# Optimization experiments

Hardware: AMD Instinct MI355X
Metric: run time of the kernel (lower is better)

Reference implementation:

```python
import jax, jax.numpy as jnp
from jax import lax
import numpy as np

B, C, H, W, O, K = 2, 64, 256, 256, 64, 3
STRIDE, DIL = 1, 1


def setup_inputs() -> dict:
    key = jax.random.key(0)
    ks = jax.random.split(key, 6)
    x = jax.random.normal(ks[0], (B, C, H, W), jnp.float32)
    # offset-predicting conv: 2*k^2 output channels (y,x per kernel tap)
    offset_w = jax.random.normal(ks[1], (2 * K * K, C, K, K), jnp.float32) * 0.01
    offset_b = jax.random.normal(ks[2], (2 * K * K,), jnp.float32) * 0.01
    # modulation conv: k^2 output channels
    amp_w = jax.random.normal(ks[3], (K * K, C, K, K), jnp.float32) * 0.01
    amp_b = jax.random.normal(ks[4], (K * K,), jnp.float32) * 0.01
    # conv3d weight [O, C, 1, 1, k^2] flattened to [O, C, k^2]
    w3d = jax.random.normal(ks[5], (O, C, K * K), jnp.float32) * (1.0 / np.sqrt(C * K * K))
    return {"x": x, "offset_w": offset_w, "offset_b": offset_b,
            "amp_w": amp_w, "amp_b": amp_b, "w3d": w3d}


def _conv2d(inp, w, b):
    out = lax.conv_general_dilated(inp, w, (STRIDE, STRIDE), 'VALID')
    return out + b[None, :, None, None]


def reference(x, offset_w, offset_b, amp_w, amp_b, w3d):
    k2 = K * K
    # 'same' padding as _pad_intput (k=3, s=1, d=1 -> pad 1 each side)
    pfs = K + (K - 1) * (DIL - 1)
    p = pfs - 1
    p0 = p // 2
    pad = jnp.pad(x, ((0, 0), (0, 0), (p0, p - p0), (p0, p - p0)))
    Bb, Cc, in_h, in_w = pad.shape

    off = _conv2d(pad, offset_w, offset_b)          # [B, 2k2, oh, ow]
    oh, ow = off.shape[2], off.shape[3]
    off = off.reshape(Bb, k2, 2, oh, ow).transpose(0, 3, 4, 1, 2)  # [B,oh,ow,k2,2]
    y_off, x_off = off[..., 0], off[..., 1]

    amp = jax.nn.sigmoid(_conv2d(pad, amp_w, amp_b))  # [B, k2, oh, ow]

    # base sampling grid (row-major over (ky,kx), as in nn.Unfold)
    ky, kx = jnp.meshgrid(jnp.arange(K), jnp.arange(K), indexing='ij')
    yb = (jnp.arange(oh) * STRIDE)[:, None] + (ky.reshape(-1) * DIL)[None, :]  # [oh,k2]
    xb = (jnp.arange(ow) * STRIDE)[:, None] + (kx.reshape(-1) * DIL)[None, :]  # [ow,k2]

    y = jnp.clip(yb[None, :, None, :].astype(jnp.float32) + y_off, 0, in_h - 1)
    xx = jnp.clip(xb[None, None, :, :].astype(jnp.float32) + x_off, 0, in_w - 1)
    y0 = jnp.floor(y)
    x0 = jnp.floor(xx)
    y1 = jnp.clip(y0 + 1, 0, in_h - 1)
    x1 = jnp.clip(x0 + 1, 0, in_w - 1)
    y0 = jnp.clip(y0, 0, in_h - 1)
    x0 = jnp.clip(x0, 0, in_w - 1)

    flat = pad.transpose(0, 2, 3, 1).reshape(Bb, in_h * in_w, Cc)

    def gather(yi, xi):
        idx = (yi.astype(jnp.int32) * in_w + xi.astype(jnp.int32)).reshape(Bb, -1)
        return jnp.take_along_axis(flat, idx[:, :, None], axis=1).reshape(Bb, oh, ow, k2, Cc)

    p0g = gather(y0, x0)
    p1g = gather(y0, x1)
    p2g = gather(y1, x0)
    p3g = gather(y1, x1)

    w0 = (y1 - y) * (x1 - xx)
    w1 = (y1 - y) * (xx - x0)
    w2 = (y - y0) * (x1 - xx)
    w3 = (y - y0) * (xx - x0)
    pixels = (w0[..., None] * p0g + w1[..., None] * p1g +
              w2[..., None] * p2g + w3[..., None] * p3g)   # [B,oh,ow,k2,C]

    # sigmoid modulation
    pixels = pixels * amp.transpose(0, 2, 3, 1)[..., None]

    # conv3d (1,1,k^2), no bias: contract over C and k^2
    out = jnp.einsum('bhwkc,ock->bohw', pixels, w3d)
    return jax.nn.relu(out)
```

## Files before the change

### kernel.cpp

```cpp
#include <hip/hip_runtime.h>
#include <hip/hip_bf16.h>
#include <math.h>

#define BB 2
#define CC 64
#define HH 256
#define WW 256
#define OO 64
#define K2 9
#define HW 65536
#define CHW (CC*HW)

typedef _Float16 h8 __attribute__((ext_vector_type(8)));
typedef __fp16 fp16x2 __attribute__((ext_vector_type(2)));
typedef __attribute__((ext_vector_type(4))) unsigned int ux4;
typedef __attribute__((ext_vector_type(4))) float f32x4;

__device__ __forceinline__ int xcd_swz(int bid, int nwg) {
    const int per = nwg >> 3;
    return (bid & 7) * per + (bid >> 3);
}
__device__ __forceinline__ unsigned short f2h(float f) {
    _Float16 h = (_Float16)f;
    return __builtin_bit_cast(unsigned short, h);
}
__device__ __forceinline__ unsigned int pkrtz(float lo, float hi) {
    fp16x2 p = __builtin_amdgcn_cvt_pkrtz(lo, hi);
    return __builtin_bit_cast(unsigned int, p);
}
__device__ __forceinline__ h8 splat8(float f) {
    _Float16 h = (_Float16)f;
    h8 r = {h, h, h, h, h, h, h, h};
    return r;
}
__device__ __forceinline__ void force(h8& v) {
    ux4 t = __builtin_bit_cast(ux4, v);
    asm volatile("" : "+v"(t));
    v = __builtin_bit_cast(h8, t);
}

__global__ __launch_bounds__(256) void k_prep(
    const float* __restrict__ offw, const float* __restrict__ ampw,
    const float* __restrict__ w3d,
    unsigned short* __restrict__ wA, unsigned short* __restrict__ wk)
{
    int i = blockIdx.x * 256 + threadIdx.x;
    if (i < 18432) {
        int ch = i / 576, sp = i % 576;
        int tap = sp >> 6, c = sp & 63;
        float v = 0.f;
        if (ch < 18)      v = offw[ch*576 + c*9 + tap];
        else if (ch < 27) v = ampw[(ch-18)*576 + c*9 + tap];
        wA[i] = f2h(v);
    } else if (i < 55296) {
        int j = i - 18432;
        int k = j >> 12, rem = j & 4095;
        int o = rem >> 6, c = rem & 63;
        wk[j] = f2h(w3d[o*576 + c*9 + k]);
    }
}

__global__ __launch_bounds__(512) void k_fused(
    const float* __restrict__ x, const unsigned short* __restrict__ wA,
    const unsigned short* __restrict__ wk,
    const float* __restrict__ offb, const float* __restrict__ ampb,
    float* __restrict__ out)
{
    __shared__ __attribute__((aligned(16))) unsigned char lds[52224];
    unsigned char* tb = lds;

    const int tid = threadIdx.x;
    const int idx = xcd_swz(blockIdx.x, BB*(HH/2)*4);
    const int wq = idx & 3, hp = (idx >> 2) & 127, b = idx >> 9;
    const int h0 = hp << 1, w0 = wq << 6;
    const int lane = tid & 63, wv = tid >> 6;
    const int lrow = lane & 15, lg = lane >> 4;

    const float* xb = x + (size_t)b * CHW;
    const int r0a = h0 - 2, c0a = w0 - 2;

    if (tid < 408) {
        const int rr = tid / 68;
        const int cc = tid - rr*68;
        const int ra = r0a + rr, ca = c0a + cc;
        const bool inb = ((unsigned)ra < 256u) && ((unsigned)ca < 256u);
        const float* ps = xb + ra*256 + ca;
        const int swz = (tid & 7) << 4;
#pragma unroll
        for (int ch = 0; ch < 64; ch += 16) {
            float v[16];
#pragma unroll
            for (int j = 0; j < 16; ++j)
                v[j] = inb ? ps[(size_t)(ch + j) * HW] : 0.f;
            ux4 q0, q1;
            q0[0] = pkrtz(v[0],  v[1]);
            q0[1] = pkrtz(v[2],  v[3]);
            q0[2] = pkrtz(v[4],  v[5]);
            q0[3] = pkrtz(v[6],  v[7]);
            q1[0] = pkrtz(v[8],  v[9]);
            q1[1] = pkrtz(v[10], v[11]);
            q1[2] = pkrtz(v[12], v[13]);
            q1[3] = pkrtz(v[14], v[15]);
            *(ux4*)(tb + tid*128 + ((ch*2     ) ^ swz)) = q0;
            *(ux4*)(tb + tid*128 + ((ch*2 + 16) ^ swz)) = q1;
        }
    }
    __syncthreads();

    unsigned int pk_oyx[K2];
    float aav[K2];
    {
        f32x4 o0 = {0.f,0.f,0.f,0.f}, o1 = {0.f,0.f,0.f,0.f};
        const int pxl = wv*16 + lrow;
        const int prow2 = pxl >> 6, pcol2 = pxl & 63;
#pragma unroll
        for (int ks = 0; ks < 18; ++ks) {
            const int sbase = ks*32 + lg*8;
            const int tap = sbase >> 6;
            const int cb  = sbase & 63;
            const int ky = tap / 3, kx = tap - ky*3;
            const int pp = (prow2 + ky + 1)*68 + pcol2 + kx + 1;
            const h8 bf = *(const h8*)(tb + pp*128 + ((2*cb) ^ ((pp & 7) << 4)));
            const h8 a0 = *(const h8*)(wA + (      lrow)*576 + sbase);
            const h8 a1 = *(const h8*)(wA + (16 + lrow)*576 + sbase);
            o0 = __builtin_amdgcn_mfma_f32_16x16x32_f16(a0, bf, o0, 0, 0, 0);
            o1 = __builtin_amdgcn_mfma_f32_16x16x32_f16(a1, bf, o1, 0, 0, 0);
        }
#pragma unroll
        for (int k = 0; k < K2; ++k) {
            const int cy = 2*k, cx = 2*k + 1, ca = 18 + k;
            const float vy = (cy < 16)
                ? __shfl(o0[cy & 3], lrow | ((cy >> 2) << 4), 64)
                : __shfl(o1[(cy - 16) & 3], lrow | (((cy - 16) >> 2) << 4), 64);
            const float vx = (cx < 16)
                ? __shfl(o0[cx & 3], lrow | ((cx >> 2) << 4), 64)
                : __shfl(o1[(cx - 16) & 3], lrow | (((cx - 16) >> 2) << 4), 64);
            const float va = __shfl(o1[(ca - 16) & 3], lrow | (((ca - 16) >> 2) << 4), 64);
            pk_oyx[k] = pkrtz(vy + offb[cy], vx + offb[cx]);
            aav[k] = 1.f / (1.f + __expf(-(va + ampb[k])));
        }
    }

    const int px = wv*16 + lrow;
    const int prow = px >> 6, pcol = px & 63;
    const int cA0 = lg*8;
    const int cA1 = 32 + lg*8;
    const int cb0 = lg*16;
    const int cb1 = 64 + lg*16;

    f32x4 acc[4];
#pragma unroll
    for (int n = 0; n < 4; ++n) acc[n] = (f32x4){0.f, 0.f, 0.f, 0.f};

#pragma unroll
    for (int k = 0; k < K2; ++k) {
        h8 bf0[4], bf1[4];
        {
            const unsigned short* wb = wk + (size_t)k*4096 + lg*8;
#pragma unroll
            for (int n = 0; n < 4; ++n) {
                bf0[n] = *(const h8*)(wb + (n*16 + lrow)*64);
                bf1[n] = *(const h8*)(wb + (n*16 + lrow)*64 + 32);
            }
        }

        const fp16x2 oyx = __builtin_bit_cast(fp16x2, pk_oyx[k]);
        const int ky = k / 3, kx = k - ky*3;
        const float aa = aav[k];
        float yy = (float)(h0 + prow + ky) + (float)oyx[0];
        float xx = (float)(w0 + pcol + kx) + (float)oyx[1];
        yy = fminf(fmaxf(yy, 0.f), 257.f);
        xx = fminf(fmaxf(xx, 0.f), 257.f);

        const float y0f = floorf(yy), x0f = floorf(xx);
        const float y1f = fminf(y0f + 1.f, 257.f);
        const float x1f = fminf(x0f + 1.f, 257.f);
        const float ay = yy - y0f, by = y1f - yy;
        const float ax = xx - x0f, bx = x1f - xx;
        const int r0 = (int)y0f - 1, r1 = (int)y1f - 1;
        const int c0 = (int)x0f - 1, c1 = (int)x1f - 1;
        const int rr0 = r0 - r0a, rr1 = r1 - r0a;
        const int cc0 = c0 - c0a, cc1 = c1 - c0a;
        const float w00 = by*bx*aa, w01 = by*ax*aa, w10 = ay*bx*aa, w11 = ay*ax*aa;

        h8 A0, A1;
        const bool ok = ((unsigned)rr0 <= 5u) && ((unsigned)rr1 <= 5u) &&
                        ((unsigned)cc0 <= 67u) && ((unsigned)cc1 <= 67u);
        if (ok) {
            const int pp00 = rr0*68 + cc0, pp01 = rr0*68 + cc1;
            const int pp10 = rr1*68 + cc0, pp11 = rr1*68 + cc1;
            const int s00 = (pp00 & 7) << 4, s01 = (pp01 & 7) << 4;
            const int s10 = (pp10 & 7) << 4, s11 = (pp11 & 7) << 4;

            h8 d00a = *(const h8*)(tb + pp00*128 + (cb0 ^ s00));
            h8 d01a = *(const h8*)(tb + pp01*128 + (cb0 ^ s01));
            h8 d10a = *(const h8*)(tb + pp10*128 + (cb0 ^ s10));
            h8 d11a = *(const h8*)(tb + pp11*128 + (cb0 ^ s11));
            h8 d00b = *(const h8*)(tb + pp00*128 + (cb1 ^ s00));
            h8 d01b = *(const h8*)(tb + pp01*128 + (cb1 ^ s01));
            h8 d10b = *(const h8*)(tb + pp10*128 + (cb1 ^ s10));
            h8 d11b = *(const h8*)(tb + pp11*128 + (cb1 ^ s11));

            force(bf0[0]); force(bf0[1]); force(bf0[2]); force(bf0[3]);
            force(bf1[0]); force(bf1[1]); force(bf1[2]); force(bf1[3]);
            force(d00a); force(d01a); force(d10a); force(d11a);
            force(d00b); force(d01b); force(d10b); force(d11b);

            const h8 Wb00 = splat8(w00), Wb01 = splat8(w01);
            const h8 Wb10 = splat8(w10), Wb11 = splat8(w11);
            h8 t = d00a * Wb00;
            t = __builtin_elementwise_fma(d01a, Wb01, t);
            t = __builtin_elementwise_fma(d10a, Wb10, t);
            t = __builtin_elementwise_fma(d11a, Wb11, t);
            A0 = t;
            h8 u = d00b * Wb00;
            u = __builtin_elementwise_fma(d01b, Wb01, u);
            u = __builtin_elementwise_fma(d10b, Wb10, u);
            u = __builtin_elementwise_fma(d11b, Wb11, u);
            A1 = u;
        } else {
            const bool vy0 = (unsigned)r0 < 256u, vy1 = (unsigned)r1 < 256u;
            const bool vx0 = (unsigned)c0 < 256u, vx1 = (unsigned)c1 < 256u;
            float W00 = w00, W01 = w01, W10 = w10, W11 = w11;
            int o00, o01, o10, o11;
            if (vy0 && vx0) o00 = r0*WW + c0; else { o00 = 0; W00 = 0.f; }
            if (vy0 && vx1) o01 = r0*WW + c1; else { o01 = 0; W01 = 0.f; }
            if (vy1 && vx0) o10 = r1*WW + c0; else { o10 = 0; W10 = 0.f; }
            if (vy1 && vx1) o11 = r1*WW + c1; else { o11 = 0; W11 = 0.f; }
            const float* pc0 = xb + (size_t)cA0 * HW;
            const float* pc1 = xb + (size_t)cA1 * HW;
#pragma unroll
            for (int jj = 0; jj < 8; ++jj) {
                float va = W00*pc0[o00] + W01*pc0[o01] + W10*pc0[o10] + W11*pc0[o11];
                pc0 += HW;
                A0[jj] = (_Float16)va;
                float vb = W00*pc1[o00] + W01*pc1[o01] + W10*pc1[o10] + W11*pc1[o11];
                pc1 += HW;
                A1[jj] = (_Float16)vb;
            }
        }

#pragma unroll
        for (int n = 0; n < 4; ++n)
            acc[n] = __builtin_amdgcn_mfma_f32_16x16x32_f16(A0, bf0[n], acc[n], 0, 0, 0);
#pragma unroll
        for (int n = 0; n < 4; ++n)
            acc[n] = __builtin_amdgcn_mfma_f32_16x16x32_f16(A1, bf1[n], acc[n], 0, 0, 0);
    }

    const int prow_s = wv >> 2;
    const int pcol_s = (wv & 3)*16 + lg*4;
    const size_t ob = (size_t)b*OO*HW + (size_t)(h0 + prow_s)*WW + w0 + pcol_s;
#pragma unroll
    for (int n = 0; n < 4; ++n) {
        f32x4 v;
        v[0] = fmaxf(acc[n][0], 0.f);
        v[1] = fmaxf(acc[n][1], 0.f);
        v[2] = fmaxf(acc[n][2], 0.f);
        v[3] = fmaxf(acc[n][3], 0.f);
        *(f32x4*)(out + ob + (size_t)(n*16 + lrow)*HW) = v;
    }
}

extern "C" void kernel_launch(void* const* d_in, const int* in_sizes, int n_in,
                              void* d_out, int out_size, void* d_ws, size_t ws_size,
                              hipStream_t stream) {
    const float* x    = (const float*)d_in[0];
    const float* offw = (const float*)d_in[1];
    const float* offb = (const float*)d_in[2];
    const float* ampw = (const float*)d_in[3];
    const float* ampb = (const float*)d_in[4];
    const float* w3d  = (const float*)d_in[5];
    float* out = (float*)d_out;

    unsigned short* wA = (unsigned short*)d_ws;
    unsigned short* wk = wA + 18432;

    k_prep<<<216, 256, 0, stream>>>(offw, ampw, w3d, wA, wk);
    k_fused<<<BB*(HH/2)*4, 512, 0, stream>>>(x, wA, wk, offb, ampb, out);
}
```

Before: 120.2 us.

## Split deformable taps across wave halves with LDS reduction, one row per block

Each block now covers one output row of 64 pixels instead of two rows. The two halves of the block's waves divide the nine sampling taps (five and four), and their partial MFMA accumulators are summed through LDS before ReLU and the store. This doubles the block count and shortens each wave's serial tap chain, aiming to improve latency hiding and occupancy. The cost is that the halo load is repeated more often, the offset and amplitude convolution is computed twice per pixel, and an extra LDS reduction with two barriers is added. The asm register-forcing helper is also removed.

```diff
diff --git a/kernel.cpp b/kernel.cpp
--- a/kernel.cpp
+++ b/kernel.cpp
@@ -32,11 +32,6 @@
     _Float16 h = (_Float16)f;
     h8 r = {h, h, h, h, h, h, h, h};
     return r;
-}
-__device__ __forceinline__ void force(h8& v) {
-    ux4 t = __builtin_bit_cast(ux4, v);
-    asm volatile("" : "+v"(t));
-    v = __builtin_bit_cast(h8, t);
 }
 
 __global__ __launch_bounds__(256) void k_prep(
@@ -66,20 +61,23 @@
     const float* __restrict__ offb, const float* __restrict__ ampb,
     float* __restrict__ out)
 {
-    __shared__ __attribute__((aligned(16))) unsigned char lds[52224];
+    __shared__ __attribute__((aligned(16))) unsigned char lds[43520];
     unsigned char* tb = lds;
+    float* red = (float*)lds;
 
     const int tid = threadIdx.x;
-    const int idx = xcd_swz(blockIdx.x, BB*(HH/2)*4);
-    const int wq = idx & 3, hp = (idx >> 2) & 127, b = idx >> 9;
-    const int h0 = hp << 1, w0 = wq << 6;
+    const int idx = xcd_swz(blockIdx.x, BB*HH*4);
+    const int wq = idx & 3, h = (idx >> 2) & 255, b = idx >> 10;
+    const int w0 = wq << 6;
     const int lane = tid & 63, wv = tid >> 6;
     const int lrow = lane & 15, lg = lane >> 4;
+    const int g = wv & 3;
+    const int half = wv >> 2;
 
     const float* xb = x + (size_t)b * CHW;
-    const int r0a = h0 - 2, c0a = w0 - 2;
-
-    if (tid < 408) {
+    const int r0a = h - 2, c0a = w0 - 2;
+
+    if (tid < 340) {
         const int rr = tid / 68;
         const int cc = tid - rr*68;
         const int ra = r0a + rr, ca = c0a + cc;
@@ -111,15 +109,14 @@
     float aav[K2];
     {
         f32x4 o0 = {0.f,0.f,0.f,0.f}, o1 = {0.f,0.f,0.f,0.f};
-        const int pxl = wv*16 + lrow;
-        const int prow2 = pxl >> 6, pcol2 = pxl & 63;
+        const int pxl = g*16 + lrow;
 #pragma unroll
         for (int ks = 0; ks < 18; ++ks) {
             const int sbase = ks*32 + lg*8;
             const int tap = sbase >> 6;
             const int cb  = sbase & 63;
             const int ky = tap / 3, kx = tap - ky*3;
-            const int pp = (prow2 + ky + 1)*68 + pcol2 + kx + 1;
+            const int pp = (ky + 1)*68 + pxl + kx + 1;
             const h8 bf = *(const h8*)(tb + pp*128 + ((2*cb) ^ ((pp & 7) << 4)));
             const h8 a0 = *(const h8*)(wA + (      lrow)*576 + sbase);
             const h8 a1 = *(const h8*)(wA + (16 + lrow)*576 + sbase);
@@ -141,8 +138,7 @@
         }
     }
 
-    const int px = wv*16 + lrow;
-    const int prow = px >> 6, pcol = px & 63;
+    const int pxl = g*16 + lrow;
     const int cA0 = lg*8;
     const int cA1 = 32 + lg*8;
     const int cb0 = lg*16;
@@ -152,8 +148,7 @@
 #pragma unroll
     for (int n = 0; n < 4; ++n) acc[n] = (f32x4){0.f, 0.f, 0.f, 0.f};
 
-#pragma unroll
-    for (int k = 0; k < K2; ++k) {
+    auto tap_body = [&](int k) {
         h8 bf0[4], bf1[4];
         {
             const unsigned short* wb = wk + (size_t)k*4096 + lg*8;
@@ -167,8 +162,8 @@
         const fp16x2 oyx = __builtin_bit_cast(fp16x2, pk_oyx[k]);
         const int ky = k / 3, kx = k - ky*3;
         const float aa = aav[k];
-        float yy = (float)(h0 + prow + ky) + (float)oyx[0];
-        float xx = (float)(w0 + pcol + kx) + (float)oyx[1];
+        float yy = (float)(h + ky) + (float)oyx[0];
+        float xx = (float)(w0 + pxl + kx) + (float)oyx[1];
         yy = fminf(fmaxf(yy, 0.f), 257.f);
         xx = fminf(fmaxf(xx, 0.f), 257.f);
 
@@ -184,30 +179,25 @@
         const float w00 = by*bx*aa, w01 = by*ax*aa, w10 = ay*bx*aa, w11 = ay*ax*aa;
 
         h8 A0, A1;
-        const bool ok = ((unsigned)rr0 <= 5u) && ((unsigned)rr1 <= 5u) &&
+        const bool ok = ((unsigned)rr0 <= 4u) && ((unsigned)rr1 <= 4u) &&
                         ((unsigned)cc0 <= 67u) && ((unsigned)cc1 <= 67u);
         if (ok) {
             const int pp00 = rr0*68 + cc0, pp01 = rr0*68 + cc1;
             const int pp10 = rr1*68 + cc0, pp11 = rr1*68 + cc1;
             const int s00 = (pp00 & 7) << 4, s01 = (pp01 & 7) << 4;
             const int s10 = (pp10 & 7) << 4, s11 = (pp11 & 7) << 4;
-
-            h8 d00a = *(const h8*)(tb + pp00*128 + (cb0 ^ s00));
-            h8 d01a = *(const h8*)(tb + pp01*128 + (cb0 ^ s01));
-            h8 d10a = *(const h8*)(tb + pp10*128 + (cb0 ^ s10));
-            h8 d11a = *(const h8*)(tb + pp11*128 + (cb0 ^ s11));
-            h8 d00b = *(const h8*)(tb + pp00*128 + (cb1 ^ s00));
-            h8 d01b = *(const h8*)(tb + pp01*128 + (cb1 ^ s01));
-            h8 d10b = *(const h8*)(tb + pp10*128 + (cb1 ^ s10));
-            h8 d11b = *(const h8*)(tb + pp11*128 + (cb1 ^ s11));
-
-            force(bf0[0]); force(bf0[1]); force(bf0[2]); force(bf0[3]);
-            force(bf1[0]); force(bf1[1]); force(bf1[2]); force(bf1[3]);
-            force(d00a); force(d01a); force(d10a); force(d11a);
-            force(d00b); force(d01b); force(d10b); force(d11b);
-
             const h8 Wb00 = splat8(w00), Wb01 = splat8(w01);
             const h8 Wb10 = splat8(w10), Wb11 = splat8(w11);
+
+            const h8 d00a = *(const h8*)(tb + pp00*128 + (cb0 ^ s00));
+            const h8 d01a = *(const h8*)(tb + pp01*128 + (cb0 ^ s01));
+            const h8 d10a = *(const h8*)(tb + pp10*128 + (cb0 ^ s10));
+            const h8 d11a = *(const h8*)(tb + pp11*128 + (cb0 ^ s11));
+            const h8 d00b = *(const h8*)(tb + pp00*128 + (cb1 ^ s00));
+            const h8 d01b = *(const h8*)(tb + pp01*128 + (cb1 ^ s01));
+            const h8 d10b = *(const h8*)(tb + pp10*128 + (cb1 ^ s10));
+            const h8 d11b = *(const h8*)(tb + pp11*128 + (cb1 ^ s11));
+
             h8 t = d00a * Wb00;
             t = __builtin_elementwise_fma(d01a, Wb01, t);
             t = __builtin_elementwise_fma(d10a, Wb10, t);
@@ -246,19 +236,36 @@
 #pragma unroll
         for (int n = 0; n < 4; ++n)
             acc[n] = __builtin_amdgcn_mfma_f32_16x16x32_f16(A1, bf1[n], acc[n], 0, 0, 0);
-    }
-
-    const int prow_s = wv >> 2;
-    const int pcol_s = (wv & 3)*16 + lg*4;
-    const size_t ob = (size_t)b*OO*HW + (size_t)(h0 + prow_s)*WW + w0 + pcol_s;
-#pragma unroll
-    for (int n = 0; n < 4; ++n) {
-        f32x4 v;
-        v[0] = fmaxf(acc[n][0], 0.f);
-        v[1] = fmaxf(acc[n][1], 0.f);
-        v[2] = fmaxf(acc[n][2], 0.f);
-        v[3] = fmaxf(acc[n][3], 0.f);
-        *(f32x4*)(out + ob + (size_t)(n*16 + lrow)*HW) = v;
+    };
+
+    if (half == 0) {
+#pragma unroll
+        for (int k = 0; k < 5; ++k) tap_body(k);
+    } else {
+#pragma unroll
+        for (int k = 5; k < K2; ++k) tap_body(k);
+    }
+
+    __syncthreads();
+    if (half == 1) {
+#pragma unroll
+        for (int n = 0; n < 4; ++n)
+#pragma unroll
+            for (int r = 0; r < 4; ++r)
+                red[(n*4 + r)*256 + g*64 + lane] = acc[n][r];
+    }
+    __syncthreads();
+
+    if (half == 0) {
+        const size_t ob = (size_t)b*OO*HW + (size_t)h*WW + w0 + g*16 + lg*4;
+#pragma unroll
+        for (int n = 0; n < 4; ++n) {
+            f32x4 v;
+#pragma unroll
+            for (int r = 0; r < 4; ++r)
+                v[r] = fmaxf(acc[n][r] + red[(n*4 + r)*256 + g*64 + lane], 0.f);
+            *(f32x4*)(out + ob + (size_t)(n*16 + lrow)*HW) = v;
+        }
     }
 }
 
@@ -277,5 +284,5 @@
     unsigned short* wk = wA + 18432;
 
     k_prep<<<216, 256, 0, stream>>>(offw, ampw, w3d, wA, wk);
-    k_fused<<<BB*(HH/2)*4, 512, 0, stream>>>(x, wA, wk, offb, ampb, out);
-}
+    k_fused<<<BB*HH*4, 512, 0, stream>>>(x, wA, wk, offb, ampb, out);
+}
```

Result: slower. 170.1 us (+41.5%).
